# Performance work log

Hardware: AMD Instinct MI355X
Metric: run time of the kernel (lower is better)

## Reference

```python
import jax, jax.numpy as jnp
import numpy as np
import math

N_EMBD = 1024
N_HEAD = 16
HEAD_DIM = N_EMBD // N_HEAD
B, T = 2, 2048
LORA_RANK = 16      # 8-bit setting
LORA_SCALE = 32.0 / 16.0  # alpha / rank
QMIN, QMAX = 0.0, 255.0   # 8-bit asymmetric


def round_ste(x):
    return x + jax.lax.stop_gradient(jnp.round(x) - x)


def fake_quant(x, scale, zero_point):
    # LearnableFakeQuantize, asymmetric 8-bit, straight-through round
    q = jnp.clip(round_ste(x / scale + zero_point), QMIN, QMAX)
    return (q - zero_point) * scale


def lora_linear(x, w, b, la, lb):
    # base linear + LoRA path (dropout disabled / eval)
    return x @ w + b + LORA_SCALE * ((x @ la) @ lb)


def setup_inputs() -> dict:
    key = jax.random.key(0)
    ks = jax.random.split(key, 10)
    std = 0.02
    hidden_states = jax.random.normal(ks[0], (B, T, N_EMBD), dtype=jnp.float32)
    w_attn = jax.random.normal(ks[1], (N_EMBD, 3 * N_EMBD), dtype=jnp.float32) * std
    b_attn = jnp.zeros((3 * N_EMBD,), dtype=jnp.float32)
    la_attn = jax.random.normal(ks[2], (N_EMBD, LORA_RANK), dtype=jnp.float32) * std
    lb_attn = jnp.zeros((LORA_RANK, 3 * N_EMBD), dtype=jnp.float32)
    w_proj = jax.random.normal(ks[3], (N_EMBD, N_EMBD), dtype=jnp.float32) * std
    b_proj = jnp.zeros((N_EMBD,), dtype=jnp.float32)
    la_proj = jax.random.normal(ks[4], (N_EMBD, LORA_RANK), dtype=jnp.float32) * std
    lb_proj = jnp.zeros((LORA_RANK, N_EMBD), dtype=jnp.float32)
    kv_scale = jnp.asarray(0.05, dtype=jnp.float32)
    kv_zero_point = jnp.asarray(128.0, dtype=jnp.float32)
    return {
        'hidden_states': hidden_states,
        'w_attn': w_attn, 'b_attn': b_attn, 'la_attn': la_attn, 'lb_attn': lb_attn,
        'w_proj': w_proj, 'b_proj': b_proj, 'la_proj': la_proj, 'lb_proj': lb_proj,
        'kv_scale': kv_scale, 'kv_zero_point': kv_zero_point,
    }


def reference(hidden_states, w_attn, b_attn, la_attn, lb_attn,
              w_proj, b_proj, la_proj, lb_proj, kv_scale, kv_zero_point):
    Bn, Tn, C = hidden_states.shape
    qkv = lora_linear(hidden_states, w_attn, b_attn, la_attn, lb_attn)
    q, k, v = jnp.split(qkv, 3, axis=2)
    # [B, T, C] -> [B, H, T, D]
    def to_heads(x):
        return x.reshape(Bn, Tn, N_HEAD, HEAD_DIM).transpose(0, 2, 1, 3)
    q, k, v = to_heads(q), to_heads(k), to_heads(v)
    k = fake_quant(k, kv_scale, kv_zero_point)
    v = fake_quant(v, kv_scale, kv_zero_point)
    scores = jnp.einsum('bhqd,bhkd->bhqk', q, k) / math.sqrt(HEAD_DIM)
    causal = jnp.tril(jnp.ones((Tn, Tn), dtype=bool))
    scores = jnp.where(causal, scores, -jnp.inf)
    attn = jax.nn.softmax(scores, axis=-1)
    out = jnp.einsum('bhqk,bhkd->bhqd', attn, v)
    out = out.transpose(0, 2, 1, 3).reshape(Bn, Tn, C)
    return lora_linear(out, w_proj, b_proj, la_proj, lb_proj)
```

## Files before the change

### kernel.cpp

```cpp
#include <hip/hip_runtime.h>
#include <hip/hip_bf16.h>
#include <math.h>

#define N_EMBD   1024
#define N_HEAD   16
#define HEAD_DIM 64
#define BATCH    2
#define TSEQ     2048
#define RANK     16
#define LORA_SCALE 2.0f
#define M_TOTAL  (BATCH * TSEQ)
#define C3       (3 * N_EMBD)

typedef unsigned short ushort_t;
typedef __attribute__((ext_vector_type(8))) short bf16x8;
typedef __attribute__((ext_vector_type(4))) float f32x4;

__device__ __forceinline__ float fake_quant(float x, float scale, float zp) {
    float q = rintf(x / scale + zp);
    q = fminf(fmaxf(q, 0.0f), 255.0f);
    return (q - zp) * scale;
}

__device__ __forceinline__ ushort_t bf16bits(float f) {
    union { __hip_bfloat16 h; ushort_t u; } c;
    c.h = __float2bfloat16(f);
    return c.u;
}

__device__ __forceinline__ float bfraw2f(ushort_t u) {
    union { unsigned int i; float f; } c; c.i = ((unsigned int)u) << 16; return c.f;
}

__global__ void cvt_split_kernel(const float* __restrict__ in,
                                 __hip_bfloat16* __restrict__ hi,
                                 __hip_bfloat16* __restrict__ lo, int n4) {
    int i = blockIdx.x * 256 + threadIdx.x;
    if (i >= n4) return;
    float4 v = ((const float4*)in)[i];
    float vs[4] = {v.x, v.y, v.z, v.w};
    #pragma unroll
    for (int k = 0; k < 4; ++k) {
        __hip_bfloat16 h = __float2bfloat16(vs[k]);
        hi[i * 4 + k] = h;
        lo[i * 4 + k] = __float2bfloat16(vs[k] - __bfloat162float(h));
    }
}

__global__ void transpose_split_kernel(const float* __restrict__ in,
                                       __hip_bfloat16* __restrict__ hiT,
                                       __hip_bfloat16* __restrict__ loT,
                                       int R, int C) {
    __shared__ float tl[32][33];
    const int c0 = blockIdx.x * 32, r0 = blockIdx.y * 32;
    const int tx = threadIdx.x & 31, ty = threadIdx.x >> 5;
    for (int i = ty; i < 32; i += 8)
        tl[i][tx] = in[(size_t)(r0 + i) * C + c0 + tx];
    __syncthreads();
    for (int i = ty; i < 32; i += 8) {
        float v = tl[tx][i];
        __hip_bfloat16 h = __float2bfloat16(v);
        size_t o = (size_t)(c0 + i) * R + r0 + tx;
        hiT[o] = h;
        if (loT) loT[o] = __float2bfloat16(v - __bfloat162float(h));
    }
}

__global__ void vtrans_kernel(const ushort_t* __restrict__ Vb,
                              ushort_t* __restrict__ Vt) {
    __shared__ ushort_t tl[64][68];
    const int bh = blockIdx.x & 31, tt = blockIdx.x >> 5;
    const int tid = threadIdx.x;
    {
        const int t = tid >> 2, d0 = (tid & 3) * 16;
        const uint4 u = *(const uint4*)(Vb + ((size_t)bh * TSEQ + tt * 64 + t) * 64 + d0);
        *(uint4*)&tl[t][d0] = u;
        *(uint4*)&tl[t][d0 + 8] = *(const uint4*)(Vb + ((size_t)bh * TSEQ + tt * 64 + t) * 64 + d0 + 8);
    }
    __syncthreads();
    const int d = tid >> 2, t0 = (tid & 3) * 16;
    unsigned int wbuf[8];
    #pragma unroll
    for (int j = 0; j < 8; ++j)
        wbuf[j] = (unsigned int)tl[t0 + 2 * j][d] | ((unsigned int)tl[t0 + 2 * j + 1][d] << 16);
    ushort_t* dst = Vt + ((size_t)bh * 64 + d) * TSEQ + tt * 64 + t0;
    *(uint4*)dst       = make_uint4(wbuf[0], wbuf[1], wbuf[2], wbuf[3]);
    *(uint4*)(dst + 8) = make_uint4(wbuf[4], wbuf[5], wbuf[6], wbuf[7]);
}

__global__ void lora_t_part_kernel(const float* __restrict__ x,
                                   const float* __restrict__ la,
                                   float* __restrict__ tpart, int K) {
    __shared__ float Xs[16][64];
    const int tid = threadIdx.x;
    const int ty = tid >> 4, tx = tid & 15;
    const int row0 = blockIdx.x * 16;
    const int kbase = blockIdx.y * 256;
    float acc = 0.0f;
    for (int k0 = kbase; k0 < kbase + 256; k0 += 64) {
        int rr = tid >> 4, kk = (tid & 15) * 4;
        float4 v = *(const float4*)(x + (size_t)(row0 + rr) * K + k0 + kk);
        Xs[rr][kk] = v.x; Xs[rr][kk + 1] = v.y; Xs[rr][kk + 2] = v.z; Xs[rr][kk + 3] = v.w;
        __syncthreads();
        for (int k = 0; k < 64; ++k)
            acc += Xs[ty][k] * la[(size_t)(k0 + k) * RANK + tx];
        __syncthreads();
    }
    tpart[((size_t)blockIdx.y * M_TOTAL + row0 + ty) * RANK + tx] = acc;
}

__global__ void lora_t_part_bf16_kernel(const ushort_t* __restrict__ x,
                                        const float* __restrict__ la,
                                        float* __restrict__ tpart, int K) {
    __shared__ float Xs[16][64];
    const int tid = threadIdx.x;
    const int ty = tid >> 4, tx = tid & 15;
    const int row0 = blockIdx.x * 16;
    const int kbase = blockIdx.y * 256;
    float acc = 0.0f;
    for (int k0 = kbase; k0 < kbase + 256; k0 += 64) {
        int rr = tid >> 4, kk = (tid & 15) * 4;
        const ushort4 u = *(const ushort4*)(x + (size_t)(row0 + rr) * K + k0 + kk);
        Xs[rr][kk] = bfraw2f(u.x); Xs[rr][kk + 1] = bfraw2f(u.y);
        Xs[rr][kk + 2] = bfraw2f(u.z); Xs[rr][kk + 3] = bfraw2f(u.w);
        __syncthreads();
        for (int k = 0; k < 64; ++k)
            acc += Xs[ty][k] * la[(size_t)(k0 + k) * RANK + tx];
        __syncthreads();
    }
    tpart[((size_t)blockIdx.y * M_TOTAL + row0 + ty) * RANK + tx] = acc;
}

__device__ __forceinline__ int sw_off(int r, int c) {
    return ((r >> 1) << 7) + (((((r & 1) << 2) | c) ^ ((r >> 1) & 7)) << 4);
}

template <bool SPLIT>
__global__ __launch_bounds__(256, 3)
void gemm_mfma_kernel(const __hip_bfloat16* __restrict__ Ah,
                      const __hip_bfloat16* __restrict__ Al,
                      const __hip_bfloat16* __restrict__ Bh,
                      const __hip_bfloat16* __restrict__ Bl,
                      const float* __restrict__ bias,
                      const float* __restrict__ tpart,
                      const float* __restrict__ lb,
                      float* __restrict__ Cf,
                      ushort_t* __restrict__ Qb,
                      ushort_t* __restrict__ Kb,
                      ushort_t* __restrict__ Vb,
                      const float* __restrict__ sp,
                      const float* __restrict__ zp,
                      int M, int N, int K, int split_col0, int out_mode) {
    constexpr int TILE = 128 * 32;
    __shared__ __hip_bfloat16 As[(SPLIT ? 2 : 1) * TILE];
    __shared__ __hip_bfloat16 Bs[(SPLIT ? 2 : 1) * TILE];
    __shared__ float Ts[128 * 16];
    __shared__ float Ls[16 * 128];

    const int tid = threadIdx.x;
    const int lane = tid & 63, w = tid >> 6;

    int bcol, brow;
    {
        const int NC = gridDim.x, NR = gridDim.y;
        const int lid = blockIdx.y * NC + blockIdx.x;
        const int xcd = lid & 7, s = lid >> 3;
        const int cw = NC >> 1, rh = NR >> 2;
        const int cg = xcd & 1, rg = xcd >> 1;
        bcol = cg * cw + (s % cw);
        brow = rg * rh + (s / cw);
    }
    const int row0 = brow * 128, col0 = bcol * 128;
    const int wr = (w >> 1) * 64, wc = (w & 1) * 64;
    const bool do_split = SPLIT && (col0 >= split_col0);

    const int s_lc = (lane & 7) ^ ((lane >> 3) & 7);
    const int s_rb = 2 * (lane >> 3) + (s_lc >> 2);
    const int s_c8 = (s_lc & 3) * 8;

    float qsc = 0.f, qzp = 0.f;
    if (out_mode == 1) { qsc = sp[0]; qzp = zp[0]; }

    f32x4 acc[4][4];
    #pragma unroll
    for (int i = 0; i < 4; ++i)
        #pragma unroll
        for (int j = 0; j < 4; ++j)
            acc[i][j] = (f32x4){0.f, 0.f, 0.f, 0.f};

    const int arow = wr + (lane & 15);
    const int chunk = lane >> 4;

    for (int k0 = 0; k0 < K; k0 += 32) {
        #pragma unroll
        for (int qq = 0; qq < 2; ++qq) {
            const int q = 2 * w + qq;
            const int r = 16 * q + s_rb;
            const __hip_bfloat16* gA = Ah + (size_t)(row0 + r) * K + k0 + s_c8;
            __builtin_amdgcn_global_load_lds(
                (const __attribute__((address_space(1))) void*)gA,
                (__attribute__((address_space(3))) void*)(As + q * 512), 16, 0, 0);
            const __hip_bfloat16* gB = Bh + (size_t)(col0 + r) * K + k0 + s_c8;
            __builtin_amdgcn_global_load_lds(
                (const __attribute__((address_space(1))) void*)gB,
                (__attribute__((address_space(3))) void*)(Bs + q * 512), 16, 0, 0);
            if (do_split) {
                const __hip_bfloat16* gAl = Al + (size_t)(row0 + r) * K + k0 + s_c8;
                __builtin_amdgcn_global_load_lds(
                    (const __attribute__((address_space(1))) void*)gAl,
                    (__attribute__((address_space(3))) void*)(As + TILE + q * 512), 16, 0, 0);
                const __hip_bfloat16* gBl = Bl + (size_t)(col0 + r) * K + k0 + s_c8;
                __builtin_amdgcn_global_load_lds(
                    (const __attribute__((address_space(1))) void*)gBl,
                    (__attribute__((address_space(3))) void*)(Bs + TILE + q * 512), 16, 0, 0);
            }
        }
        __syncthreads();

        const char* ab = (const char*)As;
        const char* bb = (const char*)Bs;
        bf16x8 a_h[4], b_h[4], a_l[4], b_l[4];
        #pragma unroll
        for (int mi = 0; mi < 4; ++mi) {
            int off = sw_off(arow + mi * 16, chunk);
            a_h[mi] = *(const bf16x8*)(ab + off);
            if (do_split) a_l[mi] = *(const bf16x8*)(ab + 2 * TILE + off);
        }
        #pragma unroll
        for (int nj = 0; nj < 4; ++nj) {
            int off = sw_off(wc + nj * 16 + (lane & 15), chunk);
            b_h[nj] = *(const bf16x8*)(bb + off);
            if (do_split) b_l[nj] = *(const bf16x8*)(bb + 2 * TILE + off);
        }
        #pragma unroll
        for (int mi = 0; mi < 4; ++mi)
            #pragma unroll
            for (int nj = 0; nj < 4; ++nj) {
                acc[mi][nj] = __builtin_amdgcn_mfma_f32_16x16x32_bf16(a_h[mi], b_h[nj], acc[mi][nj], 0, 0, 0);
                if (do_split) {
                    acc[mi][nj] = __builtin_amdgcn_mfma_f32_16x16x32_bf16(a_h[mi], b_l[nj], acc[mi][nj], 0, 0, 0);
                    acc[mi][nj] = __builtin_amdgcn_mfma_f32_16x16x32_bf16(a_l[mi], b_h[nj], acc[mi][nj], 0, 0, 0);
                }
            }
        __syncthreads();
    }

    {
        int r = tid >> 1, j0 = (tid & 1) * 8;
        float4 t0 = {0, 0, 0, 0}, t1 = {0, 0, 0, 0};
        #pragma unroll
        for (int c = 0; c < 4; ++c) {
            const float* src = tpart + ((size_t)c * M_TOTAL + row0 + r) * RANK + j0;
            float4 s0 = *(const float4*)src;
            float4 s1 = *(const float4*)(src + 4);
            t0.x += s0.x; t0.y += s0.y; t0.z += s0.z; t0.w += s0.w;
            t1.x += s1.x; t1.y += s1.y; t1.z += s1.z; t1.w += s1.w;
        }
        *(float4*)(Ts + r * 16 + j0)     = t0;
        *(float4*)(Ts + r * 16 + j0 + 4) = t1;
        int rr = tid >> 4, c0 = (tid & 15) * 8;
        const float4* lsrc = (const float4*)(lb + (size_t)rr * N + col0 + c0);
        float4* ldst = (float4*)(Ls + rr * 128 + c0);
        ldst[0] = lsrc[0]; ldst[1] = lsrc[1];
    }
    __syncthreads();
    #pragma unroll
    for (int mi = 0; mi < 4; ++mi)
        #pragma unroll
        for (int nj = 0; nj < 4; ++nj) {
            const int coll = wc + nj * 16 + (lane & 15);
            const float bv = bias[col0 + coll];
            #pragma unroll
            for (int rg = 0; rg < 4; ++rg) {
                const int rowl = wr + mi * 16 + (lane >> 4) * 4 + rg;
                float lsum = 0.f;
                #pragma unroll
                for (int rr = 0; rr < 16; ++rr)
                    lsum += Ts[rowl * 16 + rr] * Ls[rr * 128 + coll];
                const float val = acc[mi][nj][rg] + bv + LORA_SCALE * lsum;
                if (out_mode == 0) {
                    Cf[(size_t)(row0 + rowl) * N + col0 + coll] = val;
                } else {
                    const int R = row0 + rowl;
                    const int b = R >> 11, t = R & 2047;
                    const int CN = col0 + coll;
                    const int sec = CN >> 10, head = (CN >> 6) & 15, d = CN & 63;
                    const size_t off = (((size_t)(b * 16 + head)) * TSEQ + t) * 64 + d;
                    if (sec == 0)      Qb[off] = bf16bits(val * 0.125f);
                    else if (sec == 1) Kb[off] = bf16bits(fake_quant(val, qsc, qzp));
                    else               Vb[off] = bf16bits(fake_quant(val, qsc, qzp));
                }
            }
        }
}

__global__ __launch_bounds__(256)
void mfma_attn_kernel(const ushort_t* __restrict__ Qb,
                      const ushort_t* __restrict__ Kq,
                      const ushort_t* __restrict__ Vtq,
                      ushort_t* __restrict__ outb) {
    const int bx = blockIdx.x;
    const int bh = bx & 31;
    const int qt = 31 - (bx >> 5);
    const int b = bh >> 4, h = bh & 15;
    const int tid = threadIdx.x;
    const int lane = tid & 63, w = tid >> 6;
    const int m16 = lane & 15, qc = lane >> 4;
    const int m7 = m16 & 7;

    __shared__ ushort_t Qs[4096];
    __shared__ ushort_t Ks[4096];
    __shared__ ushort_t Vs[4096];
    __shared__ ushort_t Ps[4096];

    const int s_g = (lane & 7) ^ ((lane >> 3) & 7);
    const int s_r = lane >> 3;

    const ushort_t* Qg = Qb + (size_t)bh * TSEQ * 64;
    const ushort_t* Kg = Kq + (size_t)bh * TSEQ * 64;
    const ushort_t* Vg = Vtq + (size_t)bh * 64 * TSEQ;

    #pragma unroll
    for (int pp = 0; pp < 2; ++pp) {
        const int p = 2 * w + pp;
        const ushort_t* gq = Qg + ((size_t)(qt * 64 + 8 * p + s_r)) * 64 + s_g * 8;
        __builtin_amdgcn_global_load_lds(
            (const __attribute__((address_space(1))) void*)gq,
            (__attribute__((address_space(3))) void*)(Qs + p * 512), 16, 0, 0);
    }
    __syncthreads();

    bf16x8 a_q[2];
    {
        const int row = 16 * w + m16;
        #pragma unroll
        for (int c = 0; c < 2; ++c) {
            const int g = qc + 4 * c;
            a_q[c] = *(const bf16x8*)((const char*)Qs + row * 128 + ((g ^ m7) << 4));
        }
    }

    float m_st[4], l_st[4];
    f32x4 o_acc[4];
    #pragma unroll
    for (int r = 0; r < 4; ++r) { m_st[r] = -INFINITY; l_st[r] = 0.0f; }
    #pragma unroll
    for (int dj = 0; dj < 4; ++dj) o_acc[dj] = (f32x4){0.f, 0.f, 0.f, 0.f};

    for (int kt = 0; kt <= qt; ++kt) {
        __syncthreads();
        #pragma unroll
        for (int pp = 0; pp < 2; ++pp) {
            const int p = 2 * w + pp;
            const ushort_t* gk = Kg + ((size_t)(kt * 64 + 8 * p + s_r)) * 64 + s_g * 8;
            __builtin_amdgcn_global_load_lds(
                (const __attribute__((address_space(1))) void*)gk,
                (__attribute__((address_space(3))) void*)(Ks + p * 512), 16, 0, 0);
            const ushort_t* gv = Vg + ((size_t)(8 * p + s_r)) * TSEQ + kt * 64 + s_g * 8;
            __builtin_amdgcn_global_load_lds(
                (const __attribute__((address_space(1))) void*)gv,
                (__attribute__((address_space(3))) void*)(Vs + p * 512), 16, 0, 0);
        }
        __syncthreads();

        const bool diag = (kt == qt);
        const int nj_hi = diag ? (w + 1) : 4;

        f32x4 s[4];
        #pragma unroll
        for (int nj = 0; nj < 4; ++nj) s[nj] = (f32x4){0.f, 0.f, 0.f, 0.f};
        #pragma unroll
        for (int c = 0; c < 2; ++c) {
            #pragma unroll
            for (int nj = 0; nj < 4; ++nj) {
                if (nj < nj_hi) {
                    const int row = 16 * nj + m16;
                    const int g = qc + 4 * c;
                    bf16x8 bk = *(const bf16x8*)((const char*)Ks + row * 128 + ((g ^ m7) << 4));
                    s[nj] = __builtin_amdgcn_mfma_f32_16x16x32_bf16(a_q[c], bk, s[nj], 0, 0, 0);
                }
            }
        }

        float alpha[4], p_[4][4];
        #pragma unroll
        for (int reg = 0; reg < 4; ++reg) {
            const int qrow = 16 * w + 4 * qc + reg;
            float sv[4];
            float rm = -INFINITY;
            #pragma unroll
            for (int nj = 0; nj < 4; ++nj) {
                float v = s[nj][reg];
                if (diag && (m16 + 16 * nj > qrow)) v = -INFINITY;
                sv[nj] = v;
                rm = fmaxf(rm, v);
            }
            #pragma unroll
            for (int off = 1; off < 16; off <<= 1)
                rm = fmaxf(rm, __shfl_xor(rm, off, 16));
            const float mo = m_st[reg];
            const float mn = fmaxf(mo, rm);
            const float al = __expf(mo - mn);
            float rs = 0.f;
            #pragma unroll
            for (int nj = 0; nj < 4; ++nj) {
                float pv = __expf(sv[nj] - mn);
                p_[reg][nj] = pv;
                rs += pv;
            }
            #pragma unroll
            for (int off = 1; off < 16; off <<= 1)
                rs += __shfl_xor(rs, off, 16);
            l_st[reg] = al * l_st[reg] + rs;
            m_st[reg] = mn;
            alpha[reg] = al;
        }

        #pragma unroll
        for (int reg = 0; reg < 4; ++reg) {
            const int row = 16 * w + 4 * qc + reg;
            const int r7 = row & 7;
            #pragma unroll
            for (int nj = 0; nj < 4; ++nj) {
                const int k = m16 + 16 * nj;
                Ps[row * 64 + (((k >> 3) ^ r7) << 3) + (k & 7)] = bf16bits(p_[reg][nj]);
            }
        }

        #pragma unroll
        for (int dj = 0; dj < 4; ++dj)
            #pragma unroll
            for (int reg = 0; reg < 4; ++reg)
                o_acc[dj][reg] *= alpha[reg];

        const int c_hi = diag ? (w >= 2 ? 2 : 1) : 2;
        #pragma unroll
        for (int c = 0; c < 2; ++c) {
            if (c < c_hi) {
                const int rowp = 16 * w + m16;
                const int g = qc + 4 * c;
                bf16x8 ap = *(const bf16x8*)((const char*)Ps + rowp * 128 + ((g ^ m7) << 4));
                #pragma unroll
                for (int dj = 0; dj < 4; ++dj) {
                    const int rowv = 16 * dj + m16;
                    bf16x8 bv = *(const bf16x8*)((const char*)Vs + rowv * 128 + ((g ^ m7) << 4));
                    o_acc[dj] = __builtin_amdgcn_mfma_f32_16x16x32_bf16(ap, bv, o_acc[dj], 0, 0, 0);
                }
            }
        }
    }

    #pragma unroll
    for (int reg = 0; reg < 4; ++reg) {
        const float inv = 1.0f / l_st[reg];
        const int q = qt * 64 + 16 * w + 4 * qc + reg;
        #pragma unroll
        for (int dj = 0; dj < 4; ++dj) {
            const int d = m16 + 16 * dj;
            outb[((size_t)b * TSEQ + q) * N_EMBD + h * 64 + d] = bf16bits(o_acc[dj][reg] * inv);
        }
    }
}

extern "C" void kernel_launch(void* const* d_in, const int* in_sizes, int n_in,
                              void* d_out, int out_size, void* d_ws, size_t ws_size,
                              hipStream_t stream) {
    const float* x        = (const float*)d_in[0];
    const float* w_attn   = (const float*)d_in[1];
    const float* b_attn   = (const float*)d_in[2];
    const float* la_attn  = (const float*)d_in[3];
    const float* lb_attn  = (const float*)d_in[4];
    const float* w_proj   = (const float*)d_in[5];
    const float* b_proj   = (const float*)d_in[6];
    const float* la_proj  = (const float*)d_in[7];
    const float* lb_proj  = (const float*)d_in[8];
    const float* kv_scale = (const float*)d_in[9];
    const float* kv_zp    = (const float*)d_in[10];
    float* out = (float*)d_out;

    char* ws = (char*)d_ws;
    float* t_attn_p       = (float*)ws;          ws += (size_t)4 * M_TOTAL * RANK * 4;
    float* t_proj_p       = (float*)ws;          ws += (size_t)4 * M_TOTAL * RANK * 4;
    ushort_t* aob         = (ushort_t*)ws;       ws += (size_t)M_TOTAL * N_EMBD * 2;
    __hip_bfloat16* x_hi  = (__hip_bfloat16*)ws; ws += (size_t)M_TOTAL * N_EMBD * 2;
    __hip_bfloat16* x_lo  = (__hip_bfloat16*)ws; ws += (size_t)M_TOTAL * N_EMBD * 2;
    __hip_bfloat16* wqT_h = (__hip_bfloat16*)ws; ws += (size_t)C3 * N_EMBD * 2;
    __hip_bfloat16* wqT_l = (__hip_bfloat16*)ws; ws += (size_t)C3 * N_EMBD * 2;
    __hip_bfloat16* wpT   = (__hip_bfloat16*)ws; ws += (size_t)N_EMBD * N_EMBD * 2;
    ushort_t* Qb          = (ushort_t*)ws;       ws += (size_t)32 * TSEQ * 64 * 2;
    ushort_t* Kb          = (ushort_t*)ws;       ws += (size_t)32 * TSEQ * 64 * 2;
    ushort_t* Vb          = (ushort_t*)ws;       ws += (size_t)32 * TSEQ * 64 * 2;
    ushort_t* Vtq         = (ushort_t*)ws;       ws += (size_t)32 * 64 * TSEQ * 2;

    cvt_split_kernel<<<dim3(M_TOTAL * N_EMBD / 4 / 256), 256, 0, stream>>>(
        x, x_hi, x_lo, M_TOTAL * N_EMBD / 4);
    transpose_split_kernel<<<dim3(C3 / 32, N_EMBD / 32), 256, 0, stream>>>(
        w_attn, wqT_h, wqT_l, N_EMBD, C3);
    transpose_split_kernel<<<dim3(N_EMBD / 32, N_EMBD / 32), 256, 0, stream>>>(
        w_proj, wpT, nullptr, N_EMBD, N_EMBD);
    lora_t_part_kernel<<<dim3(M_TOTAL / 16, 4), 256, 0, stream>>>(x, la_attn, t_attn_p, N_EMBD);

    gemm_mfma_kernel<true><<<dim3(C3 / 128, M_TOTAL / 128), 256, 0, stream>>>(
        x_hi, x_lo, wqT_h, wqT_l, b_attn, t_attn_p, lb_attn,
        nullptr, Qb, Kb, Vb, kv_scale, kv_zp,
        M_TOTAL, C3, N_EMBD, 2 * N_EMBD, 1);

    vtrans_kernel<<<dim3(32 * (TSEQ / 64)), 256, 0, stream>>>(Vb, Vtq);

    mfma_attn_kernel<<<dim3(32 * 32), 256, 0, stream>>>(Qb, Kb, Vtq, aob);

    lora_t_part_bf16_kernel<<<dim3(M_TOTAL / 16, 4), 256, 0, stream>>>(aob, la_proj, t_proj_p, N_EMBD);

    gemm_mfma_kernel<false><<<dim3(N_EMBD / 128, M_TOTAL / 128), 256, 0, stream>>>(
        (const __hip_bfloat16*)aob, nullptr, wpT, nullptr, b_proj, t_proj_p, lb_proj,
        out, nullptr, nullptr, nullptr, nullptr, nullptr,
        M_TOTAL, N_EMBD, N_EMBD, 1 << 30, 0);
}
```

Before: 347.5 us.

## Fuse prep kernels, process two key tiles per attention step, use exp2 softmax

Folds the x hi/lo bf16 split into the LoRA down-projection kernel and merges the two weight-transpose launches into one, which removes a kernel launch and one full pass over x. The attention kernel now loads two 64-key tiles of K and V per iteration with doubled LDS buffers, so it synchronises half as often. It also writes P straight into LDS, reusing the Q staging buffer once Q is in registers. Q is pre-scaled by log2(e)/sqrt(d) so the softmax can use exp2f. This raises LDS use and register pressure and does extra masked work on partially causal tiles.

```diff
diff --git a/kernel.cpp b/kernel.cpp
--- a/kernel.cpp
+++ b/kernel.cpp
@@ -11,6 +11,7 @@
 #define LORA_SCALE 2.0f
 #define M_TOTAL  (BATCH * TSEQ)
 #define C3       (3 * N_EMBD)
+#define QSCALE   0.18033688f
 
 typedef unsigned short ushort_t;
 typedef __attribute__((ext_vector_type(8))) short bf16x8;
@@ -32,27 +33,16 @@
     union { unsigned int i; float f; } c; c.i = ((unsigned int)u) << 16; return c.f;
 }
 
-__global__ void cvt_split_kernel(const float* __restrict__ in,
-                                 __hip_bfloat16* __restrict__ hi,
-                                 __hip_bfloat16* __restrict__ lo, int n4) {
-    int i = blockIdx.x * 256 + threadIdx.x;
-    if (i >= n4) return;
-    float4 v = ((const float4*)in)[i];
-    float vs[4] = {v.x, v.y, v.z, v.w};
-    #pragma unroll
-    for (int k = 0; k < 4; ++k) {
-        __hip_bfloat16 h = __float2bfloat16(vs[k]);
-        hi[i * 4 + k] = h;
-        lo[i * 4 + k] = __float2bfloat16(vs[k] - __bfloat162float(h));
-    }
-}
-
-__global__ void transpose_split_kernel(const float* __restrict__ in,
-                                       __hip_bfloat16* __restrict__ hiT,
-                                       __hip_bfloat16* __restrict__ loT,
-                                       int R, int C) {
+__global__ void transpose_both_kernel(const float* __restrict__ w_attn,
+                                      const float* __restrict__ w_proj,
+                                      __hip_bfloat16* __restrict__ wqT_h,
+                                      __hip_bfloat16* __restrict__ wqT_l,
+                                      __hip_bfloat16* __restrict__ wpT) {
     __shared__ float tl[32][33];
-    const int c0 = blockIdx.x * 32, r0 = blockIdx.y * 32;
+    const float* in; __hip_bfloat16* hiT; __hip_bfloat16* loT; int R, C, cx;
+    if (blockIdx.x < 96) { in = w_attn; hiT = wqT_h; loT = wqT_l; R = N_EMBD; C = C3; cx = blockIdx.x; }
+    else                 { in = w_proj; hiT = wpT;   loT = nullptr; R = N_EMBD; C = N_EMBD; cx = blockIdx.x - 96; }
+    const int c0 = cx * 32, r0 = blockIdx.y * 32;
     const int tx = threadIdx.x & 31, ty = threadIdx.x >> 5;
     for (int i = ty; i < 32; i += 8)
         tl[i][tx] = in[(size_t)(r0 + i) * C + c0 + tx];
@@ -90,7 +80,9 @@
 
 __global__ void lora_t_part_kernel(const float* __restrict__ x,
                                    const float* __restrict__ la,
-                                   float* __restrict__ tpart, int K) {
+                                   float* __restrict__ tpart,
+                                   __hip_bfloat16* __restrict__ hi,
+                                   __hip_bfloat16* __restrict__ lo, int K) {
     __shared__ float Xs[16][64];
     const int tid = threadIdx.x;
     const int ty = tid >> 4, tx = tid & 15;
@@ -99,8 +91,20 @@
     float acc = 0.0f;
     for (int k0 = kbase; k0 < kbase + 256; k0 += 64) {
         int rr = tid >> 4, kk = (tid & 15) * 4;
-        float4 v = *(const float4*)(x + (size_t)(row0 + rr) * K + k0 + kk);
+        const size_t goff = (size_t)(row0 + rr) * K + k0 + kk;
+        float4 v = *(const float4*)(x + goff);
         Xs[rr][kk] = v.x; Xs[rr][kk + 1] = v.y; Xs[rr][kk + 2] = v.z; Xs[rr][kk + 3] = v.w;
+        float vs[4] = {v.x, v.y, v.z, v.w};
+        ushort4 uh, ul;
+        ushort_t* uhp = (ushort_t*)&uh; ushort_t* ulp = (ushort_t*)&ul;
+        #pragma unroll
+        for (int q = 0; q < 4; ++q) {
+            ushort_t hb = bf16bits(vs[q]);
+            uhp[q] = hb;
+            ulp[q] = bf16bits(vs[q] - bfraw2f(hb));
+        }
+        *(ushort4*)((ushort_t*)hi + goff) = uh;
+        *(ushort4*)((ushort_t*)lo + goff) = ul;
         __syncthreads();
         for (int k = 0; k < 64; ++k)
             acc += Xs[ty][k] * la[(size_t)(k0 + k) * RANK + tx];
@@ -286,7 +290,7 @@
                     const int CN = col0 + coll;
                     const int sec = CN >> 10, head = (CN >> 6) & 15, d = CN & 63;
                     const size_t off = (((size_t)(b * 16 + head)) * TSEQ + t) * 64 + d;
-                    if (sec == 0)      Qb[off] = bf16bits(val * 0.125f);
+                    if (sec == 0)      Qb[off] = bf16bits(val * QSCALE);
                     else if (sec == 1) Kb[off] = bf16bits(fake_quant(val, qsc, qzp));
                     else               Vb[off] = bf16bits(fake_quant(val, qsc, qzp));
                 }
@@ -308,10 +312,10 @@
     const int m16 = lane & 15, qc = lane >> 4;
     const int m7 = m16 & 7;
 
-    __shared__ ushort_t Qs[4096];
-    __shared__ ushort_t Ks[4096];
-    __shared__ ushort_t Vs[4096];
-    __shared__ ushort_t Ps[4096];
+    __shared__ ushort_t QP[4096];
+    __shared__ ushort_t Ps1[4096];
+    __shared__ ushort_t Ks[8192];
+    __shared__ ushort_t Vs[8192];
 
     const int s_g = (lane & 7) ^ ((lane >> 3) & 7);
     const int s_r = lane >> 3;
@@ -326,7 +330,7 @@
         const ushort_t* gq = Qg + ((size_t)(qt * 64 + 8 * p + s_r)) * 64 + s_g * 8;
         __builtin_amdgcn_global_load_lds(
             (const __attribute__((address_space(1))) void*)gq,
-            (__attribute__((address_space(3))) void*)(Qs + p * 512), 16, 0, 0);
+            (__attribute__((address_space(3))) void*)(QP + p * 512), 16, 0, 0);
     }
     __syncthreads();
 
@@ -336,9 +340,10 @@
         #pragma unroll
         for (int c = 0; c < 2; ++c) {
             const int g = qc + 4 * c;
-            a_q[c] = *(const bf16x8*)((const char*)Qs + row * 128 + ((g ^ m7) << 4));
-        }
-    }
+            a_q[c] = *(const bf16x8*)((const char*)QP + row * 128 + ((g ^ m7) << 4));
+        }
+    }
+    __syncthreads();
 
     float m_st[4], l_st[4];
     f32x4 o_acc[4];
@@ -347,51 +352,54 @@
     #pragma unroll
     for (int dj = 0; dj < 4; ++dj) o_acc[dj] = (f32x4){0.f, 0.f, 0.f, 0.f};
 
-    for (int kt = 0; kt <= qt; ++kt) {
-        __syncthreads();
-        #pragma unroll
-        for (int pp = 0; pp < 2; ++pp) {
-            const int p = 2 * w + pp;
-            const ushort_t* gk = Kg + ((size_t)(kt * 64 + 8 * p + s_r)) * 64 + s_g * 8;
+    const int npairs = (qt + 2) >> 1;
+    for (int p2 = 0; p2 < npairs; ++p2) {
+        const int kb = p2 * 128;
+        __syncthreads();
+        #pragma unroll
+        for (int pp = 0; pp < 4; ++pp) {
+            const int tt = pp & 1;
+            const int g8 = 2 * w + (pp >> 1);
+            const ushort_t* gk = Kg + ((size_t)(kb + tt * 64 + 8 * g8 + s_r)) * 64 + s_g * 8;
             __builtin_amdgcn_global_load_lds(
                 (const __attribute__((address_space(1))) void*)gk,
-                (__attribute__((address_space(3))) void*)(Ks + p * 512), 16, 0, 0);
-            const ushort_t* gv = Vg + ((size_t)(8 * p + s_r)) * TSEQ + kt * 64 + s_g * 8;
+                (__attribute__((address_space(3))) void*)(Ks + tt * 4096 + g8 * 512), 16, 0, 0);
+            const ushort_t* gv = Vg + ((size_t)(8 * g8 + s_r)) * TSEQ + kb + tt * 64 + s_g * 8;
             __builtin_amdgcn_global_load_lds(
                 (const __attribute__((address_space(1))) void*)gv,
-                (__attribute__((address_space(3))) void*)(Vs + p * 512), 16, 0, 0);
-        }
-        __syncthreads();
-
-        const bool diag = (kt == qt);
-        const int nj_hi = diag ? (w + 1) : 4;
-
-        f32x4 s[4];
-        #pragma unroll
-        for (int nj = 0; nj < 4; ++nj) s[nj] = (f32x4){0.f, 0.f, 0.f, 0.f};
+                (__attribute__((address_space(3))) void*)(Vs + tt * 4096 + g8 * 512), 16, 0, 0);
+        }
+        __syncthreads();
+
+        const int kmaxw = qt * 64 + 16 * w + 15 - kb;
+
+        f32x4 s[8];
+        #pragma unroll
+        for (int nj = 0; nj < 8; ++nj) s[nj] = (f32x4){0.f, 0.f, 0.f, 0.f};
         #pragma unroll
         for (int c = 0; c < 2; ++c) {
             #pragma unroll
-            for (int nj = 0; nj < 4; ++nj) {
-                if (nj < nj_hi) {
-                    const int row = 16 * nj + m16;
+            for (int nj = 0; nj < 8; ++nj) {
+                if (16 * nj <= kmaxw) {
+                    const int row = 16 * (nj & 3) + m16;
                     const int g = qc + 4 * c;
-                    bf16x8 bk = *(const bf16x8*)((const char*)Ks + row * 128 + ((g ^ m7) << 4));
+                    bf16x8 bk = *(const bf16x8*)((const char*)Ks + (nj >> 2) * 8192 + row * 128 + ((g ^ m7) << 4));
                     s[nj] = __builtin_amdgcn_mfma_f32_16x16x32_bf16(a_q[c], bk, s[nj], 0, 0, 0);
                 }
             }
         }
 
-        float alpha[4], p_[4][4];
+        float alpha[4];
         #pragma unroll
         for (int reg = 0; reg < 4; ++reg) {
             const int qrow = 16 * w + 4 * qc + reg;
-            float sv[4];
+            const int dq = qt * 64 + qrow - kb;
+            float sv[8];
             float rm = -INFINITY;
             #pragma unroll
-            for (int nj = 0; nj < 4; ++nj) {
+            for (int nj = 0; nj < 8; ++nj) {
                 float v = s[nj][reg];
-                if (diag && (m16 + 16 * nj > qrow)) v = -INFINITY;
+                if (m16 + 16 * nj > dq) v = -INFINITY;
                 sv[nj] = v;
                 rm = fmaxf(rm, v);
             }
@@ -400,13 +408,16 @@
                 rm = fmaxf(rm, __shfl_xor(rm, off, 16));
             const float mo = m_st[reg];
             const float mn = fmaxf(mo, rm);
-            const float al = __expf(mo - mn);
+            const float al = exp2f(mo - mn);
             float rs = 0.f;
-            #pragma unroll
-            for (int nj = 0; nj < 4; ++nj) {
-                float pv = __expf(sv[nj] - mn);
-                p_[reg][nj] = pv;
+            const int r7 = qrow & 7;
+            #pragma unroll
+            for (int nj = 0; nj < 8; ++nj) {
+                float pv = exp2f(sv[nj] - mn);
                 rs += pv;
+                const int k = m16 + 16 * (nj & 3);
+                ushort_t* Pdst = (nj < 4) ? QP : Ps1;
+                Pdst[qrow * 64 + (((k >> 3) ^ r7) << 3) + (k & 7)] = bf16bits(pv);
             }
             #pragma unroll
             for (int off = 1; off < 16; off <<= 1)
@@ -417,33 +428,23 @@
         }
 
         #pragma unroll
-        for (int reg = 0; reg < 4; ++reg) {
-            const int row = 16 * w + 4 * qc + reg;
-            const int r7 = row & 7;
-            #pragma unroll
-            for (int nj = 0; nj < 4; ++nj) {
-                const int k = m16 + 16 * nj;
-                Ps[row * 64 + (((k >> 3) ^ r7) << 3) + (k & 7)] = bf16bits(p_[reg][nj]);
-            }
-        }
-
-        #pragma unroll
         for (int dj = 0; dj < 4; ++dj)
             #pragma unroll
             for (int reg = 0; reg < 4; ++reg)
                 o_acc[dj][reg] *= alpha[reg];
 
-        const int c_hi = diag ? (w >= 2 ? 2 : 1) : 2;
-        #pragma unroll
-        for (int c = 0; c < 2; ++c) {
-            if (c < c_hi) {
-                const int rowp = 16 * w + m16;
-                const int g = qc + 4 * c;
-                bf16x8 ap = *(const bf16x8*)((const char*)Ps + rowp * 128 + ((g ^ m7) << 4));
+        const int rowp = 16 * w + m16;
+        const int r7p = rowp & 7;
+        #pragma unroll
+        for (int c = 0; c < 4; ++c) {
+            if (32 * c <= kmaxw) {
+                const int g = qc + 4 * (c & 1);
+                const ushort_t* Psrc = (c < 2) ? QP : Ps1;
+                bf16x8 ap = *(const bf16x8*)((const char*)Psrc + rowp * 128 + ((g ^ r7p) << 4));
                 #pragma unroll
                 for (int dj = 0; dj < 4; ++dj) {
                     const int rowv = 16 * dj + m16;
-                    bf16x8 bv = *(const bf16x8*)((const char*)Vs + rowv * 128 + ((g ^ m7) << 4));
+                    bf16x8 bv = *(const bf16x8*)((const char*)Vs + (c >> 1) * 8192 + rowv * 128 + ((g ^ m7) << 4));
                     o_acc[dj] = __builtin_amdgcn_mfma_f32_16x16x32_bf16(ap, bv, o_acc[dj], 0, 0, 0);
                 }
             }
@@ -492,13 +493,10 @@
     ushort_t* Vb          = (ushort_t*)ws;       ws += (size_t)32 * TSEQ * 64 * 2;
     ushort_t* Vtq         = (ushort_t*)ws;       ws += (size_t)32 * 64 * TSEQ * 2;
 
-    cvt_split_kernel<<<dim3(M_TOTAL * N_EMBD / 4 / 256), 256, 0, stream>>>(
-        x, x_hi, x_lo, M_TOTAL * N_EMBD / 4);
-    transpose_split_kernel<<<dim3(C3 / 32, N_EMBD / 32), 256, 0, stream>>>(
-        w_attn, wqT_h, wqT_l, N_EMBD, C3);
-    transpose_split_kernel<<<dim3(N_EMBD / 32, N_EMBD / 32), 256, 0, stream>>>(
-        w_proj, wpT, nullptr, N_EMBD, N_EMBD);
-    lora_t_part_kernel<<<dim3(M_TOTAL / 16, 4), 256, 0, stream>>>(x, la_attn, t_attn_p, N_EMBD);
+    transpose_both_kernel<<<dim3(128, 32), 256, 0, stream>>>(
+        w_attn, w_proj, wqT_h, wqT_l, wpT);
+    lora_t_part_kernel<<<dim3(M_TOTAL / 16, 4), 256, 0, stream>>>(
+        x, la_attn, t_attn_p, x_hi, x_lo, N_EMBD);
 
     gemm_mfma_kernel<true><<<dim3(C3 / 128, M_TOTAL / 128), 256, 0, stream>>>(
         x_hi, x_lo, wqT_h, wqT_l, b_attn, t_attn_p, lb_attn,
```

Result: slower. 462.2 us (+33.0%).
